# Performance work log

Hardware: AMD Instinct MI355X
Metric: run time of the kernel (lower is better)

Reference implementation:

```python
import jax, jax.numpy as jnp
import numpy as np

D_MODEL = 512
N_PAIRS = D_MODEL // 2
B, T = 8, 4096


def setup_inputs() -> dict:
    key = jax.random.key(0)
    ks = jax.random.split(key, 7)
    scale = 1.0 / np.sqrt(D_MODEL)
    return {
        "x_seq": jax.random.normal(ks[0], (B, T, D_MODEL), dtype=jnp.float32),
        "W_angle": jax.random.uniform(ks[1], (D_MODEL, N_PAIRS), jnp.float32, -scale, scale),
        "b_angle": jnp.zeros((N_PAIRS,), jnp.float32),
        "W_decay": jax.random.uniform(ks[2], (D_MODEL, 1), jnp.float32, -scale, scale),
        "b_decay": jnp.full((1,), 1.4, jnp.float32),
        "W_input": jax.random.uniform(ks[3], (D_MODEL, D_MODEL), jnp.float32, -scale, scale),
        "b_input": jax.random.uniform(ks[4], (D_MODEL,), jnp.float32, -scale, scale),
    }


def _givens_ssm(x_seq, W_angle, b_angle, W_decay, b_decay, W_input, b_input):
    Bb, Tt, D = x_seq.shape
    P = D // 2
    angles = jnp.einsum("btd,dp->btp", x_seq, W_angle) + b_angle          # [B,T,P]
    decays = jax.nn.sigmoid(jnp.einsum("btd,dk->btk", x_seq, W_decay) + b_decay)[..., 0]  # [B,T]
    inj = jnp.einsum("btd,de->bte", x_seq, W_input) + b_input              # [B,T,D]
    inj = inj.reshape(Bb, Tt, P, 2)

    # scan over time: h_t = decay_t * Rot(angles_t) h_{t-1} + inj_t, pairwise 2x2 rotations
    def step(h, inp):
        a, d, u = inp  # a:[B,P], d:[B], u:[B,P,2]
        c, s = jnp.cos(a), jnp.sin(a)
        he = c * h[..., 0] - s * h[..., 1]
        ho = s * h[..., 0] + c * h[..., 1]
        h_new = d[:, None, None] * jnp.stack([he, ho], axis=-1) + u
        return h_new, h_new

    h0 = jnp.zeros((Bb, P, 2), x_seq.dtype)
    xs = (jnp.swapaxes(angles, 0, 1), jnp.swapaxes(decays, 0, 1), jnp.swapaxes(inj, 0, 1))
    _, states = jax.lax.scan(step, h0, xs)  # [T,B,P,2]
    return jnp.swapaxes(states, 0, 1).reshape(Bb, Tt, D)


def reference(x_seq, W_angle, b_angle, W_decay, b_decay, W_input, b_input):
    return _givens_ssm(x_seq, W_angle, b_angle, W_decay, b_decay, W_input, b_input)
```

## Files before the change

kernel.cpp:

```cpp
#include <hip/hip_runtime.h>
#include <math.h>

typedef _Float16 half_t;
typedef __attribute__((ext_vector_type(8))) _Float16 half8;
typedef __attribute__((ext_vector_type(4))) _Float16 half4;
typedef __attribute__((ext_vector_type(2))) _Float16 half2v;
typedef __attribute__((ext_vector_type(4))) float floatx4;

#define BATCH   8
#define SEQ     4096
#define DM      512
#define NP      256
#define M_TOT   32768
#define NTOT    768
#define CHUNKS  256
#define CHUNK_LEN 16

__device__ __forceinline__ void async_load16(const void* g, void* l) {
    __builtin_amdgcn_global_load_lds((const __attribute__((address_space(1))) void*)g,
                                     (__attribute__((address_space(3))) void*)l,
                                     16, 0, 0);
}

__global__ __launch_bounds__(256) void decay_convert(const float* __restrict__ X,
                                                     const float* __restrict__ Wd,
                                                     const float* __restrict__ bd,
                                                     float* __restrict__ dec,
                                                     half_t* __restrict__ Xh) {
    const int wave = threadIdx.x >> 6;
    const int lane = threadIdx.x & 63;
    const int row0 = blockIdx.x * 8 + wave * 2;
    const float4* x0 = (const float4*)(X + (size_t)row0 * DM);
    const float4* x1 = x0 + 128;
    const float4* wd = (const float4*)Wd;
    float4 a0 = x0[2 * lane], a1 = x0[2 * lane + 1];
    float4 b0 = x1[2 * lane], b1 = x1[2 * lane + 1];
    float4 w0 = wd[2 * lane], w1 = wd[2 * lane + 1];
    float s0 = a0.x * w0.x + a0.y * w0.y + a0.z * w0.z + a0.w * w0.w
             + a1.x * w1.x + a1.y * w1.y + a1.z * w1.z + a1.w * w1.w;
    float s1 = b0.x * w0.x + b0.y * w0.y + b0.z * w0.z + b0.w * w0.w
             + b1.x * w1.x + b1.y * w1.y + b1.z * w1.z + b1.w * w1.w;
    half8 h0 = {(half_t)a0.x, (half_t)a0.y, (half_t)a0.z, (half_t)a0.w,
                (half_t)a1.x, (half_t)a1.y, (half_t)a1.z, (half_t)a1.w};
    half8 h1 = {(half_t)b0.x, (half_t)b0.y, (half_t)b0.z, (half_t)b0.w,
                (half_t)b1.x, (half_t)b1.y, (half_t)b1.z, (half_t)b1.w};
    *(half8*)(Xh + (size_t)row0 * DM + lane * 8) = h0;
    *(half8*)(Xh + (size_t)(row0 + 1) * DM + lane * 8) = h1;
#pragma unroll
    for (int off = 32; off > 0; off >>= 1) {
        s0 += __shfl_down(s0, off, 64);
        s1 += __shfl_down(s1, off, 64);
    }
    if (lane == 0) {
        dec[row0]     = 1.0f / (1.0f + __expf(-(s0 + bd[0])));
        dec[row0 + 1] = 1.0f / (1.0f + __expf(-(s1 + bd[0])));
    }
}

__global__ __launch_bounds__(256) void wcat_transpose(const float* __restrict__ Wi,
                                                      const float* __restrict__ Wa,
                                                      half_t* __restrict__ Wt) {
    const int idx = blockIdx.x * 256 + threadIdx.x;
    const int n = idx >> 9;
    const int k = idx & 511;
    float v = (n < DM) ? Wi[(size_t)k * DM + n] : Wa[(size_t)k * NP + (n - DM)];
    Wt[idx] = (half_t)v;
}

__global__ __launch_bounds__(256) void gemm_fused(const half_t* __restrict__ Xh,
                                                  const half_t* __restrict__ Wt,
                                                  const float* __restrict__ bi,
                                                  const float* __restrict__ ba,
                                                  half_t* __restrict__ inj,
                                                  half_t* __restrict__ angles) {
    __shared__ __align__(16) char As[8192];
    __shared__ __align__(16) char Bs[8192];

    const int bm   = blockIdx.x;
    const int bn   = blockIdx.y;
    const int tid  = threadIdx.x;
    const int wave = tid >> 6;
    const int lane = tid & 63;
    const int quad = lane >> 4;
    const int l16  = lane & 15;
    const int wrow = wave >> 1;
    const int wcol = wave & 1;

    floatx4 acc[4][4];
#pragma unroll
    for (int i = 0; i < 4; ++i)
#pragma unroll
        for (int j = 0; j < 4; ++j) acc[i][j] = (floatx4){0.f, 0.f, 0.f, 0.f};

    const int s0 = wave * 128 + lane;
    const int s1 = s0 + 64;
    const int r0 = s0 >> 2, kql0 = (s0 & 3) ^ ((r0 >> 1) & 3);
    const int r1 = s1 >> 2, kql1 = (s1 & 3) ^ ((r1 >> 1) & 3);
    const half_t* gA0 = Xh + (size_t)(bm * 128 + r0) * DM + kql0 * 8;
    const half_t* gA1 = Xh + (size_t)(bm * 128 + r1) * DM + kql1 * 8;
    const half_t* gB0 = Wt + (size_t)(bn * 128 + r0) * DM + kql0 * 8;
    const half_t* gB1 = Wt + (size_t)(bn * 128 + r1) * DM + kql1 * 8;
    char* lA0 = As + wave * 2048;
    char* lA1 = As + wave * 2048 + 1024;
    char* lB0 = Bs + wave * 2048;
    char* lB1 = Bs + wave * 2048 + 1024;

    for (int k0 = 0; k0 < DM; k0 += 32) {
        async_load16(gA0 + k0, lA0);
        async_load16(gA1 + k0, lA1);
        async_load16(gB0 + k0, lB0);
        async_load16(gB1 + k0, lB1);
        __syncthreads();

        half8 af[4], bf[4];
#pragma unroll
        for (int mt = 0; mt < 4; ++mt) {
            const int r = wrow * 64 + mt * 16 + l16;
            af[mt] = *(const half8*)(As + r * 64 + ((quad ^ ((r >> 1) & 3)) << 4));
        }
#pragma unroll
        for (int nt = 0; nt < 4; ++nt) {
            const int r = wcol * 64 + nt * 16 + l16;
            bf[nt] = *(const half8*)(Bs + r * 64 + ((quad ^ ((r >> 1) & 3)) << 4));
        }
#pragma unroll
        for (int mt = 0; mt < 4; ++mt)
#pragma unroll
            for (int nt = 0; nt < 4; ++nt)
                acc[mt][nt] = __builtin_amdgcn_mfma_f32_16x16x32_f16(af[mt], bf[nt],
                                                                     acc[mt][nt], 0, 0, 0);
        __syncthreads();
    }

    const bool  is_inj = (bn < 4);
    half_t*     dst    = is_inj ? inj    : angles;
    const int   ldd    = is_inj ? DM     : NP;
    const int   cb     = is_inj ? bn * 128 : bn * 128 - DM;

    float bias[4];
#pragma unroll
    for (int nt = 0; nt < 4; ++nt) {
        const int colt = wcol * 64 + nt * 16 + l16;
        bias[nt] = is_inj ? bi[bn * 128 + colt] : ba[bn * 128 + colt - DM];
    }

    half_t* Cs = (half_t*)As;
#pragma unroll
    for (int rh = 0; rh < 2; ++rh) {
        __syncthreads();
        if (wrow == rh) {
#pragma unroll
            for (int mt = 0; mt < 4; ++mt)
#pragma unroll
                for (int nt = 0; nt < 4; ++nt)
#pragma unroll
                    for (int r = 0; r < 4; ++r) {
                        const int lr = mt * 16 + quad * 4 + r;
                        const int lc = wcol * 64 + nt * 16 + l16;
                        Cs[lr * 128 + lc] = (half_t)(acc[mt][nt][r] + bias[nt]);
                    }
        }
        __syncthreads();
#pragma unroll
        for (int it = 0; it < 4; ++it) {
            const int idx = it * 256 + tid;
            const int rr  = idx >> 4;
            const int cc  = (idx & 15) * 8;
            const int grow = bm * 128 + rh * 64 + rr;
            half8 v = *(half8*)(Cs + rr * 128 + cc);
            *(half8*)(dst + (size_t)grow * ldd + cb + cc) = v;
        }
    }
}

__global__ __launch_bounds__(256) void scan_sum1(const half_t* __restrict__ angles,
                                                 const float* __restrict__ decays,
                                                 const half_t* __restrict__ inj,
                                                 float* __restrict__ thetaC,
                                                 float4* __restrict__ hend,
                                                 float* __restrict__ Dprod) {
    const int b   = blockIdx.x >> 7;
    const int sub = threadIdx.x >> 7;
    const int th  = threadIdx.x & 127;
    const int c   = (blockIdx.x & 127) * 2 + sub;
    const int p0  = th * 2;
    const int t0  = c * CHUNK_LEN;

    const half_t* ap = angles + (size_t)(b * SEQ + t0) * NP + p0;
    const half4*  up = (const half4*)(inj + (size_t)(b * SEQ + t0) * DM) + th;
    const float*  dp = decays + b * SEQ + t0;

    half2v ab[2][8]; half4 ub[2][8]; float db[2][8];
#pragma unroll
    for (int j = 0; j < 8; ++j) {
        ab[0][j] = *(const half2v*)(ap + (size_t)j * NP);
        ub[0][j] = up[(size_t)j * 128];
        db[0][j] = dp[j];
    }

    float h0a = 0, h1a = 0, h0b = 0, h1b = 0, tha = 0, thb = 0, dc = 1.0f;
#pragma unroll
    for (int g = 0; g < 2; ++g) {
        const int cur = g & 1, nxt = cur ^ 1;
        if (g < 1) {
#pragma unroll
            for (int j = 0; j < 8; ++j) {
                const int t = (g + 1) * 8 + j;
                ab[nxt][j] = *(const half2v*)(ap + (size_t)t * NP);
                ub[nxt][j] = up[(size_t)t * 128];
                db[nxt][j] = dp[t];
            }
        }
#pragma unroll
        for (int j = 0; j < 8; ++j) {
            float a0 = (float)ab[cur][j][0], a1 = (float)ab[cur][j][1];
            half4 uh = ub[cur][j];
            float d  = db[cur][j];
            float s0, c0, s1, c1;
            __sincosf(a0, &s0, &c0);
            __sincosf(a1, &s1, &c1);
            float n0a = fmaf(d, c0 * h0a - s0 * h1a, (float)uh[0]);
            float n1a = fmaf(d, s0 * h0a + c0 * h1a, (float)uh[1]);
            float n0b = fmaf(d, c1 * h0b - s1 * h1b, (float)uh[2]);
            float n1b = fmaf(d, s1 * h0b + c1 * h1b, (float)uh[3]);
            h0a = n0a; h1a = n1a; h0b = n0b; h1b = n1b;
            tha += a0; thb += a1; dc *= d;
        }
    }
    const size_t cbase = (size_t)(b * CHUNKS + c) * NP + p0;
    *(float2*)(thetaC + cbase) = make_float2(tha, thb);
    hend[cbase >> 1] = make_float4(h0a, h1a, h0b, h1b);
    if (th == 0) Dprod[b * CHUNKS + c] = dc;
}

__global__ __launch_bounds__(256) void scan_chunks(const float* __restrict__ thetaC,
                                                   const float4* __restrict__ hend,
                                                   const float* __restrict__ Dprod,
                                                   float4* __restrict__ hentry) {
    const int b  = blockIdx.x >> 7;
    const int pp = blockIdx.x & 127;
    const int c  = threadIdx.x;

    __shared__ float  sTa[256], sTb[256], sD[256];
    __shared__ float4 sV[256];

    const size_t idx = (size_t)(b * CHUNKS + c);
    const float2 th2 = *(const float2*)(thetaC + idx * NP + pp * 2);
    float4 v = hend[idx * 128 + pp];
    float  D = Dprod[idx];
    float tha = th2.x, thb = th2.y;

    sTa[c] = tha; sTb[c] = thb; sD[c] = D; sV[c] = v;

#pragma unroll
    for (int o = 1; o < 256; o <<= 1) {
        __syncthreads();
        float lta = 0.f, ltb = 0.f, lD = 0.f;
        float4 lv = make_float4(0.f, 0.f, 0.f, 0.f);
        const bool has = (c >= o);
        if (has) { lta = sTa[c - o]; ltb = sTb[c - o]; lD = sD[c - o]; lv = sV[c - o]; }
        __syncthreads();
        if (has) {
            float s0, c0, s1, c1;
            __sincosf(tha, &s0, &c0);
            __sincosf(thb, &s1, &c1);
            v.x = fmaf(D, c0 * lv.x - s0 * lv.y, v.x);
            v.y = fmaf(D, s0 * lv.x + c0 * lv.y, v.y);
            v.z = fmaf(D, c1 * lv.z - s1 * lv.w, v.z);
            v.w = fmaf(D, s1 * lv.z + c1 * lv.w, v.w);
            tha += lta; thb += ltb; D *= lD;
            sTa[c] = tha; sTb[c] = thb; sD[c] = D; sV[c] = v;
        }
    }
    __syncthreads();
    const float4 e = (c == 0) ? make_float4(0.f, 0.f, 0.f, 0.f) : sV[c - 1];
    hentry[idx * 128 + pp] = e;
}

__global__ __launch_bounds__(256) void scan_final(const half_t* __restrict__ angles,
                                                  const float* __restrict__ decays,
                                                  const half_t* __restrict__ inj,
                                                  const float4* __restrict__ hentry,
                                                  float* __restrict__ out) {
    const int b   = blockIdx.x >> 7;
    const int sub = threadIdx.x >> 7;
    const int th  = threadIdx.x & 127;
    const int c   = (blockIdx.x & 127) * 2 + sub;
    const int p0  = th * 2;
    const int t0  = c * CHUNK_LEN;

    const half_t* ap = angles + (size_t)(b * SEQ + t0) * NP + p0;
    const half4*  up = (const half4*)(inj + (size_t)(b * SEQ + t0) * DM) + th;
    float4*       op = (float4*)out + (size_t)(b * SEQ + t0) * 128 + (p0 >> 1);
    const float*  dp = decays + b * SEQ + t0;

    float4 v = hentry[(size_t)(b * CHUNKS + c) * 128 + (p0 >> 1)];
    float h0a = v.x, h1a = v.y, h0b = v.z, h1b = v.w;

    half2v ab[2][8]; half4 ub[2][8]; float db[2][8];
#pragma unroll
    for (int j = 0; j < 8; ++j) {
        ab[0][j] = *(const half2v*)(ap + (size_t)j * NP);
        ub[0][j] = up[(size_t)j * 128];
        db[0][j] = dp[j];
    }

#pragma unroll
    for (int g = 0; g < 2; ++g) {
        const int cur = g & 1, nxt = cur ^ 1;
        if (g < 1) {
#pragma unroll
            for (int j = 0; j < 8; ++j) {
                const int t = (g + 1) * 8 + j;
                ab[nxt][j] = *(const half2v*)(ap + (size_t)t * NP);
                ub[nxt][j] = up[(size_t)t * 128];
                db[nxt][j] = dp[t];
            }
        }
#pragma unroll
        for (int j = 0; j < 8; ++j) {
            const int t = g * 8 + j;
            float a0 = (float)ab[cur][j][0], a1 = (float)ab[cur][j][1];
            half4 uh = ub[cur][j];
            float d  = db[cur][j];
            float s0, c0, s1, c1;
            __sincosf(a0, &s0, &c0);
            __sincosf(a1, &s1, &c1);
            float n0a = fmaf(d, c0 * h0a - s0 * h1a, (float)uh[0]);
            float n1a = fmaf(d, s0 * h0a + c0 * h1a, (float)uh[1]);
            float n0b = fmaf(d, c1 * h0b - s1 * h1b, (float)uh[2]);
            float n1b = fmaf(d, s1 * h0b + c1 * h1b, (float)uh[3]);
            h0a = n0a; h1a = n1a; h0b = n0b; h1b = n1b;
            op[(size_t)t * 128] = make_float4(h0a, h1a, h0b, h1b);
        }
    }
}

extern "C" void kernel_launch(void* const* d_in, const int* in_sizes, int n_in,
                              void* d_out, int out_size, void* d_ws, size_t ws_size,
                              hipStream_t stream) {
    const float* x  = (const float*)d_in[0];
    const float* Wa = (const float*)d_in[1];
    const float* ba = (const float*)d_in[2];
    const float* Wd = (const float*)d_in[3];
    const float* bd = (const float*)d_in[4];
    const float* Wi = (const float*)d_in[5];
    const float* bi = (const float*)d_in[6];
    float* out = (float*)d_out;

    char* ws = (char*)d_ws;
    half_t* x_h     = (half_t*)(ws);
    float*  thetaC  = (float*)(ws);
    float4* hend    = (float4*)(ws + 2097152);
    float*  Dprod   = (float*)(ws + 6291456);
    float4* hentry  = (float4*)(ws + 6299648);
    half_t* inj_h   = (half_t*)(ws + 33554432);
    half_t* angles  = (half_t*)(ws + 67108864);
    float*  decays  = (float*)(ws + 83886080);
    half_t* Wcat_t  = (half_t*)(ws + 84017152);

    decay_convert<<<M_TOT / 8, 256, 0, stream>>>(x, Wd, bd, decays, x_h);
    wcat_transpose<<<(NTOT * DM) / 256, 256, 0, stream>>>(Wi, Wa, Wcat_t);
    gemm_fused<<<dim3(M_TOT / 128, NTOT / 128), 256, 0, stream>>>(x_h, Wcat_t, bi, ba, inj_h, angles);

    scan_sum1<<<BATCH * CHUNKS / 2, 256, 0, stream>>>(angles, decays, inj_h, thetaC, hend, Dprod);
    scan_chunks<<<BATCH * 128, 256, 0, stream>>>(thetaC, hend, Dprod, hentry);
    scan_final<<<BATCH * CHUNKS / 2, 256, 0, stream>>>(angles, decays, inj_h, hentry, out);
}
```

Baseline: 203.3 us.

## Halve scan chunk length to double parallelism and swizzle GEMM epilogue LDS

Cuts the chunk length of the chunked scan from 16 to 8 and doubles the number of chunks, so the two per-chunk scan kernels launch twice as many blocks with shorter serial chains. The cross-chunk scan kernel grows to 512 threads and one more log step, and its intermediate buffers double in size. Separately, the GEMM epilogue's staging writes to shared memory use an XOR swizzle on the column index to reduce LDS bank conflicts. The trade-off is more inter-chunk scan work and workspace traffic in exchange for shorter sequential dependency chains.

```diff
diff --git a/kernel.cpp b/kernel.cpp
--- a/kernel.cpp
+++ b/kernel.cpp
@@ -13,8 +13,8 @@
 #define NP      256
 #define M_TOT   32768
 #define NTOT    768
-#define CHUNKS  256
-#define CHUNK_LEN 16
+#define CHUNKS  512
+#define CHUNK_LEN 8
 
 __device__ __forceinline__ void async_load16(const void* g, void* l) {
     __builtin_amdgcn_global_load_lds((const __attribute__((address_space(1))) void*)g,
@@ -157,7 +157,8 @@
                     for (int r = 0; r < 4; ++r) {
                         const int lr = mt * 16 + quad * 4 + r;
                         const int lc = wcol * 64 + nt * 16 + l16;
-                        Cs[lr * 128 + lc] = (half_t)(acc[mt][nt][r] + bias[nt]);
+                        Cs[lr * 128 + (lc ^ (((lr >> 2) & 3) << 4))] =
+                            (half_t)(acc[mt][nt][r] + bias[nt]);
                     }
         }
         __syncthreads();
@@ -167,7 +168,7 @@
             const int rr  = idx >> 4;
             const int cc  = (idx & 15) * 8;
             const int grow = bm * 128 + rh * 64 + rr;
-            half8 v = *(half8*)(Cs + rr * 128 + cc);
+            half8 v = *(half8*)(Cs + rr * 128 + (cc ^ (((rr >> 2) & 3) << 4)));
             *(half8*)(dst + (size_t)grow * ldd + cb + cc) = v;
         }
     }
@@ -179,10 +180,10 @@
                                                  float* __restrict__ thetaC,
                                                  float4* __restrict__ hend,
                                                  float* __restrict__ Dprod) {
-    const int b   = blockIdx.x >> 7;
+    const int b   = blockIdx.x >> 8;
     const int sub = threadIdx.x >> 7;
     const int th  = threadIdx.x & 127;
-    const int c   = (blockIdx.x & 127) * 2 + sub;
+    const int c   = (blockIdx.x & 255) * 2 + sub;
     const int p0  = th * 2;
     const int t0  = c * CHUNK_LEN;
 
@@ -190,42 +191,28 @@
     const half4*  up = (const half4*)(inj + (size_t)(b * SEQ + t0) * DM) + th;
     const float*  dp = decays + b * SEQ + t0;
 
-    half2v ab[2][8]; half4 ub[2][8]; float db[2][8];
+    half2v a[8]; half4 u[8]; float d[8];
 #pragma unroll
     for (int j = 0; j < 8; ++j) {
-        ab[0][j] = *(const half2v*)(ap + (size_t)j * NP);
-        ub[0][j] = up[(size_t)j * 128];
-        db[0][j] = dp[j];
+        a[j] = *(const half2v*)(ap + (size_t)j * NP);
+        u[j] = up[(size_t)j * 128];
+        d[j] = dp[j];
     }
 
     float h0a = 0, h1a = 0, h0b = 0, h1b = 0, tha = 0, thb = 0, dc = 1.0f;
 #pragma unroll
-    for (int g = 0; g < 2; ++g) {
-        const int cur = g & 1, nxt = cur ^ 1;
-        if (g < 1) {
-#pragma unroll
-            for (int j = 0; j < 8; ++j) {
-                const int t = (g + 1) * 8 + j;
-                ab[nxt][j] = *(const half2v*)(ap + (size_t)t * NP);
-                ub[nxt][j] = up[(size_t)t * 128];
-                db[nxt][j] = dp[t];
-            }
-        }
-#pragma unroll
-        for (int j = 0; j < 8; ++j) {
-            float a0 = (float)ab[cur][j][0], a1 = (float)ab[cur][j][1];
-            half4 uh = ub[cur][j];
-            float d  = db[cur][j];
-            float s0, c0, s1, c1;
-            __sincosf(a0, &s0, &c0);
-            __sincosf(a1, &s1, &c1);
-            float n0a = fmaf(d, c0 * h0a - s0 * h1a, (float)uh[0]);
-            float n1a = fmaf(d, s0 * h0a + c0 * h1a, (float)uh[1]);
-            float n0b = fmaf(d, c1 * h0b - s1 * h1b, (float)uh[2]);
-            float n1b = fmaf(d, s1 * h0b + c1 * h1b, (float)uh[3]);
-            h0a = n0a; h1a = n1a; h0b = n0b; h1b = n1b;
-            tha += a0; thb += a1; dc *= d;
-        }
+    for (int j = 0; j < 8; ++j) {
+        float a0 = (float)a[j][0], a1 = (float)a[j][1];
+        float dd = d[j];
+        float s0, c0, s1, c1;
+        __sincosf(a0, &s0, &c0);
+        __sincosf(a1, &s1, &c1);
+        float n0a = fmaf(dd, c0 * h0a - s0 * h1a, (float)u[j][0]);
+        float n1a = fmaf(dd, s0 * h0a + c0 * h1a, (float)u[j][1]);
+        float n0b = fmaf(dd, c1 * h0b - s1 * h1b, (float)u[j][2]);
+        float n1b = fmaf(dd, s1 * h0b + c1 * h1b, (float)u[j][3]);
+        h0a = n0a; h1a = n1a; h0b = n0b; h1b = n1b;
+        tha += a0; thb += a1; dc *= dd;
     }
     const size_t cbase = (size_t)(b * CHUNKS + c) * NP + p0;
     *(float2*)(thetaC + cbase) = make_float2(tha, thb);
@@ -233,7 +220,7 @@
     if (th == 0) Dprod[b * CHUNKS + c] = dc;
 }
 
-__global__ __launch_bounds__(256) void scan_chunks(const float* __restrict__ thetaC,
+__global__ __launch_bounds__(512) void scan_chunks(const float* __restrict__ thetaC,
                                                    const float4* __restrict__ hend,
                                                    const float* __restrict__ Dprod,
                                                    float4* __restrict__ hentry) {
@@ -241,8 +228,8 @@
     const int pp = blockIdx.x & 127;
     const int c  = threadIdx.x;
 
-    __shared__ float  sTa[256], sTb[256], sD[256];
-    __shared__ float4 sV[256];
+    __shared__ float  sTa[512], sTb[512], sD[512];
+    __shared__ float4 sV[512];
 
     const size_t idx = (size_t)(b * CHUNKS + c);
     const float2 th2 = *(const float2*)(thetaC + idx * NP + pp * 2);
@@ -253,7 +240,7 @@
     sTa[c] = tha; sTb[c] = thb; sD[c] = D; sV[c] = v;
 
 #pragma unroll
-    for (int o = 1; o < 256; o <<= 1) {
+    for (int o = 1; o < 512; o <<= 1) {
         __syncthreads();
         float lta = 0.f, ltb = 0.f, lD = 0.f;
         float4 lv = make_float4(0.f, 0.f, 0.f, 0.f);
@@ -282,10 +269,10 @@
                                                   const half_t* __restrict__ inj,
                                                   const float4* __restrict__ hentry,
                                                   float* __restrict__ out) {
-    const int b   = blockIdx.x >> 7;
+    const int b   = blockIdx.x >> 8;
     const int sub = threadIdx.x >> 7;
     const int th  = threadIdx.x & 127;
-    const int c   = (blockIdx.x & 127) * 2 + sub;
+    const int c   = (blockIdx.x & 255) * 2 + sub;
     const int p0  = th * 2;
     const int t0  = c * CHUNK_LEN;
 
@@ -297,42 +284,27 @@
     float4 v = hentry[(size_t)(b * CHUNKS + c) * 128 + (p0 >> 1)];
     float h0a = v.x, h1a = v.y, h0b = v.z, h1b = v.w;
 
-    half2v ab[2][8]; half4 ub[2][8]; float db[2][8];
+    half2v a[8]; half4 u[8]; float d[8];
 #pragma unroll
     for (int j = 0; j < 8; ++j) {
-        ab[0][j] = *(const half2v*)(ap + (size_t)j * NP);
-        ub[0][j] = up[(size_t)j * 128];
-        db[0][j] = dp[j];
-    }
-
-#pragma unroll
-    for (int g = 0; g < 2; ++g) {
-        const int cur = g & 1, nxt = cur ^ 1;
-        if (g < 1) {
-#pragma unroll
-            for (int j = 0; j < 8; ++j) {
-                const int t = (g + 1) * 8 + j;
-                ab[nxt][j] = *(const half2v*)(ap + (size_t)t * NP);
-                ub[nxt][j] = up[(size_t)t * 128];
-                db[nxt][j] = dp[t];
-            }
-        }
-#pragma unroll
-        for (int j = 0; j < 8; ++j) {
-            const int t = g * 8 + j;
-            float a0 = (float)ab[cur][j][0], a1 = (float)ab[cur][j][1];
-            half4 uh = ub[cur][j];
-            float d  = db[cur][j];
-            float s0, c0, s1, c1;
-            __sincosf(a0, &s0, &c0);
-            __sincosf(a1, &s1, &c1);
-            float n0a = fmaf(d, c0 * h0a - s0 * h1a, (float)uh[0]);
-            float n1a = fmaf(d, s0 * h0a + c0 * h1a, (float)uh[1]);
-            float n0b = fmaf(d, c1 * h0b - s1 * h1b, (float)uh[2]);
-            float n1b = fmaf(d, s1 * h0b + c1 * h1b, (float)uh[3]);
-            h0a = n0a; h1a = n1a; h0b = n0b; h1b = n1b;
-            op[(size_t)t * 128] = make_float4(h0a, h1a, h0b, h1b);
-        }
+        a[j] = *(const half2v*)(ap + (size_t)j * NP);
+        u[j] = up[(size_t)j * 128];
+        d[j] = dp[j];
+    }
+
+#pragma unroll
+    for (int j = 0; j < 8; ++j) {
+        float a0 = (float)a[j][0], a1 = (float)a[j][1];
+        float dd = d[j];
+        float s0, c0, s1, c1;
+        __sincosf(a0, &s0, &c0);
+        __sincosf(a1, &s1, &c1);
+        float n0a = fmaf(dd, c0 * h0a - s0 * h1a, (float)u[j][0]);
+        float n1a = fmaf(dd, s0 * h0a + c0 * h1a, (float)u[j][1]);
+        float n0b = fmaf(dd, c1 * h0b - s1 * h1b, (float)u[j][2]);
+        float n1b = fmaf(dd, s1 * h0b + c1 * h1b, (float)u[j][3]);
+        h0a = n0a; h1a = n1a; h0b = n0b; h1b = n1b;
+        op[(size_t)j * 128] = make_float4(h0a, h1a, h0b, h1b);
     }
 }
 
@@ -351,9 +323,9 @@
     char* ws = (char*)d_ws;
     half_t* x_h     = (half_t*)(ws);
     float*  thetaC  = (float*)(ws);
-    float4* hend    = (float4*)(ws + 2097152);
-    float*  Dprod   = (float*)(ws + 6291456);
-    float4* hentry  = (float4*)(ws + 6299648);
+    float4* hend    = (float4*)(ws + 4194304);
+    float*  Dprod   = (float*)(ws + 12582912);
+    float4* hentry  = (float4*)(ws + 12599296);
     half_t* inj_h   = (half_t*)(ws + 33554432);
     half_t* angles  = (half_t*)(ws + 67108864);
     float*  decays  = (float*)(ws + 83886080);
@@ -364,6 +336,6 @@
     gemm_fused<<<dim3(M_TOT / 128, NTOT / 128), 256, 0, stream>>>(x_h, Wcat_t, bi, ba, inj_h, angles);
 
     scan_sum1<<<BATCH * CHUNKS / 2, 256, 0, stream>>>(angles, decays, inj_h, thetaC, hend, Dprod);
-    scan_chunks<<<BATCH * 128, 256, 0, stream>>>(thetaC, hend, Dprod, hentry);
+    scan_chunks<<<BATCH * 128, 512, 0, stream>>>(thetaC, hend, Dprod, hentry);
     scan_final<<<BATCH * CHUNKS / 2, 256, 0, stream>>>(angles, decays, inj_h, hentry, out);
 }
```

Result: slower. 214.7 us (+5.6%).
